# Kernel optimization log

Measured on AMD Instinct MI355X. Metric: run time of the kernel, lower is better.

The kernel has to match this reference:

```python
import jax, jax.numpy as jnp
import numpy as np

B, N, C, H, HD, HH, WW, K, ALPHA = 8, 4096, 256, 8, 32, 64, 64, 5, 4.0


def setup_inputs() -> dict:
    key = jax.random.key(0)
    ks = jax.random.split(key, 6)
    return {
        "x": jax.random.normal(ks[0], (B, N, C), jnp.float32),
        "W_qg": jax.random.normal(ks[1], (C, 2 * C), jnp.float32) * 0.02,
        "W_kv": jax.random.normal(ks[2], (C, 2 * C), jnp.float32) * 0.02,
        "W_proj": jax.random.normal(ks[3], (C, C), jnp.float32) * 0.02,
        "b_proj": jnp.zeros((C,), jnp.float32),
        "dwc_w": jax.random.normal(ks[4], (HD, 1, K, K), jnp.float32) * 0.05,
        "dwc_b": jnp.zeros((HD,), jnp.float32),
        "power_p": jnp.zeros((1, H, 1, HD), jnp.float32),
    }


def _safe_pow(x, p):
    # x >= 0 (post-relu). 0**p == 0 for p > 0; guard base so grads stay finite.
    xs = jnp.where(x > 0, x, 1.0)
    return jnp.where(x > 0, xs ** p, 0.0)


def reference(x, W_qg, W_kv, W_proj, b_proj, dwc_w, dwc_b, power_p):
    qg = x @ W_qg                                  # (B,N,2C)
    q, g = qg[..., :C], qg[..., C:]
    kv = x @ W_kv                                  # (B,N,2C)
    k = kv[..., :C].reshape(B, N, H, HD).transpose(0, 2, 1, 3)   # (B,H,N,hd)
    v = kv[..., C:].reshape(B, N, H, HD).transpose(0, 2, 1, 3)
    q = q.reshape(B, N, H, HD).transpose(0, 2, 1, 3)

    power = 1.0 + ALPHA * jax.nn.sigmoid(power_p)  # (1,H,1,hd)
    # x_s = q_pos@kv_s + q_neg@kv_s = (q_pos+q_neg)@kv_s, kv_s = (k_pos+k_neg)^T v_s
    q_sum = _safe_pow(jax.nn.relu(q), power) + _safe_pow(jax.nn.relu(-q), power)
    k_sum = _safe_pow(jax.nn.relu(k), power) + _safe_pow(jax.nn.relu(-k), power)

    v_s, v_o = v[..., : HD // 2], v[..., HD // 2 :]
    kv_s = jnp.einsum('bhnd,bhne->bhde', k_sum, v_s)
    kv_o = jnp.einsum('bhnd,bhne->bhde', k_sum, v_o)
    x_s = jnp.einsum('bhnd,bhde->bhne', q_sum, kv_s)
    x_o = jnp.einsum('bhnd,bhde->bhne', q_sum, kv_o)
    x_att = jnp.concatenate([x_s, x_o], -1).transpose(0, 2, 1, 3).reshape(B, N, C)

    # depthwise conv branch: exact layout replication of torch permute/reshape chain
    v_img = v.transpose(0, 2, 1, 3).reshape(B * H, HD, HH, WW)
    pad = K // 2
    v_loc = jax.lax.conv_general_dilated(
        v_img, dwc_w, (1, 1), [(pad, pad), (pad, pad)],
        feature_group_count=HD,
        dimension_numbers=('NCHW', 'OIHW', 'NCHW')) + dwc_b[None, :, None, None]
    v_loc = v_loc.reshape(B, H, HD, N).transpose(0, 2, 1, 3).reshape(B, C, N).transpose(0, 2, 1)

    return ((x_att + v_loc) * g) @ W_proj + b_proj
```

## Files before the change

kernel.cpp:

```cpp
#include <hip/hip_runtime.h>
#include <hip/hip_bf16.h>
#include <math.h>

#define B_ 8
#define N_ 4096
#define C_ 256
#define H_ 8
#define HD_ 32
#define BN_ (B_ * N_)
#define E_ ((size_t)BN_ * C_)

typedef __attribute__((ext_vector_type(8))) short short8;
typedef __attribute__((ext_vector_type(4))) float f32x4;

__device__ __forceinline__ float b2f(__hip_bfloat16 x) { return __bfloat162float(x); }

__device__ __forceinline__ void gl_lds16(const void* gp, void* lp) {
    __builtin_amdgcn_global_load_lds(
        (const __attribute__((address_space(1))) unsigned int*)gp,
        (__attribute__((address_space(3))) unsigned int*)lp,
        16, 0, 0);
}

__device__ __forceinline__ float fast_abspow(float v, float p) {
    float av = fabsf(v);
    return (av > 0.f) ? __builtin_amdgcn_exp2f(p * __builtin_amdgcn_logf(av)) : 0.f;
}

__device__ __forceinline__ float bf_lo(unsigned u) { return __uint_as_float(u << 16); }
__device__ __forceinline__ float bf_hi(unsigned u) { return __uint_as_float(u & 0xffff0000u); }
__device__ __forceinline__ unsigned short f2bfbits(float f) {
    __hip_bfloat16 h = __float2bfloat16(f);
    return *(unsigned short*)&h;
}
__device__ __forceinline__ unsigned pack2(float lo, float hi) {
    return (unsigned)f2bfbits(lo) | ((unsigned)f2bfbits(hi) << 16);
}

__global__ __launch_bounds__(256) void cvt_all(
    const float* __restrict__ x, const float* __restrict__ Wqg,
    const float* __restrict__ Wkv, const float* __restrict__ Wp,
    const float* __restrict__ pp,
    __hip_bfloat16* __restrict__ xb, __hip_bfloat16* __restrict__ Wt1,
    __hip_bfloat16* __restrict__ Wt2, float* __restrict__ powers)
{
    int t = threadIdx.x;
    int bid0 = blockIdx.x;
    if (bid0 < 4096) {
        size_t i = ((size_t)bid0 * 256 + t) * 8;
        float4 a = *(const float4*)&x[i];
        float4 b = *(const float4*)&x[i + 4];
        uint4 o = {pack2(a.x, a.y), pack2(a.z, a.w), pack2(b.x, b.y), pack2(b.z, b.w)};
        *(uint4*)&xb[i] = o;
        return;
    }
    int bid = bid0 - 4096;
    if (bid == 80) {
        powers[t] = 1.0f + 4.0f / (1.0f + expf(-pp[t]));
        return;
    }
    __shared__ float tile[64][65];
    const float* src;
    __hip_bfloat16* dst;
    int scols, tr, tc, dn0;
    if (bid < 32)      { src = Wqg; scols = 512; tr = bid >> 3;        tc = bid & 7;        dst = Wt1; dn0 = tc * 64; }
    else if (bid < 64) { src = Wkv; scols = 512; tr = (bid - 32) >> 3; tc = (bid - 32) & 7; dst = Wt1; dn0 = 512 + tc * 64; }
    else               { src = Wp;  scols = 256; tr = (bid - 64) >> 2; tc = (bid - 64) & 3; dst = Wt2; dn0 = tc * 64; }
    int tx = t & 63, ty = t >> 6;
    #pragma unroll
    for (int i = 0; i < 16; i++) {
        int r = ty + i * 4;
        tile[r][tx] = src[(size_t)(tr * 64 + r) * scols + tc * 64 + tx];
    }
    __syncthreads();
    #pragma unroll
    for (int i = 0; i < 16; i++) {
        int n_local = ty + i * 4;
        dst[(size_t)(dn0 + n_local) * 256 + tr * 64 + tx] = __float2bfloat16(tile[tx][n_local]);
    }
}

__global__ __launch_bounds__(256) void gemm1_mfma(
    const __hip_bfloat16* __restrict__ xb, const __hip_bfloat16* __restrict__ Wt1,
    const float* __restrict__ powers,
    __hip_bfloat16* __restrict__ q16, __hip_bfloat16* __restrict__ k16,
    __hip_bfloat16* __restrict__ g16, __hip_bfloat16* __restrict__ v16)
{
    __shared__ __align__(16) unsigned short As[2 * 128 * 32];
    __shared__ __align__(16) unsigned short Bs[2 * 128 * 32];
    int t = threadIdx.x;
    int w = t >> 6, l = t & 63;
    int row0 = blockIdx.x * 128;
    int col0 = blockIdx.y * 128;
    int wm = (w >> 1) * 64, wn = (w & 1) * 64;
    int lane15 = l & 15, quad = l >> 4;
    int srow = l >> 2;
    int skcol = (l & 3) * 8;

    f32x4 acc[4][4];
    #pragma unroll
    for (int mi = 0; mi < 4; mi++)
        #pragma unroll
        for (int ni = 0; ni < 4; ni++) acc[mi][ni] = (f32x4){0.f, 0.f, 0.f, 0.f};

    for (int k0 = 0; k0 < 256; k0 += 64) {
        #pragma unroll
        for (int kh = 0; kh < 2; kh++) {
            #pragma unroll
            for (int i = 0; i < 2; i++) {
                int r = i * 64 + w * 16 + srow;
                int kc = k0 + kh * 32 + skcol;
                gl_lds16(&xb[(size_t)(row0 + r) * 256 + kc],
                         &As[kh * 4096 + (i * 64 + w * 16) * 32]);
                gl_lds16(&Wt1[(size_t)(col0 + r) * 256 + kc],
                         &Bs[kh * 4096 + (i * 64 + w * 16) * 32]);
            }
        }
        __syncthreads();
        #pragma unroll
        for (int kh = 0; kh < 2; kh++) {
            short8 a[4], b[4];
            #pragma unroll
            for (int mi = 0; mi < 4; mi++)
                a[mi] = *(const short8*)&As[kh * 4096 + (wm + mi * 16 + lane15) * 32 + quad * 8];
            #pragma unroll
            for (int ni = 0; ni < 4; ni++)
                b[ni] = *(const short8*)&Bs[kh * 4096 + (wn + ni * 16 + lane15) * 32 + quad * 8];
            #pragma unroll
            for (int mi = 0; mi < 4; mi++)
                #pragma unroll
                for (int ni = 0; ni < 4; ni++)
                    acc[mi][ni] = __builtin_amdgcn_mfma_f32_16x16x32_bf16(a[mi], b[ni], acc[mi][ni], 0, 0, 0);
        }
        __syncthreads();
    }

    int region = blockIdx.y >> 1;
    bool dopow = (region == 0) || (region == 2);
    __hip_bfloat16* dst = (region == 0) ? q16 : (region == 1) ? g16 : (region == 2) ? k16 : v16;
    #pragma unroll
    for (int mi = 0; mi < 4; mi++) {
        #pragma unroll
        for (int ni = 0; ni < 4; ni++) {
            int row = row0 + wm + mi * 16 + quad * 4;
            int col = col0 + wn + ni * 16 + lane15;
            int c255 = col & 255;
            float p = powers[c255];
            #pragma unroll
            for (int r = 0; r < 4; r++) {
                float v = acc[mi][ni][r];
                float o = dopow ? fast_abspow(v, p) : v;
                dst[(size_t)(row + r) * 256 + c255] = __float2bfloat16(o);
            }
        }
    }
}

__global__ __launch_bounds__(256) void kvmat_kernel(
    const __hip_bfloat16* __restrict__ k16, const __hip_bfloat16* __restrict__ v16,
    float* __restrict__ kv_part)
{
    __shared__ __align__(16) unsigned short Kl[16 * 256];
    __shared__ __align__(16) unsigned short Vl[16 * 256];
    int t = threadIdx.x;
    int bid = blockIdx.x;
    int b = bid >> 5, seg = bid & 31;
    int h = t >> 5;
    float acc[32];
    #pragma unroll
    for (int e = 0; e < 32; e++) acc[e] = 0.f;
    const size_t base = (size_t)b * N_ * 256;
    int row = t >> 4, colb = (t & 15) * 16;
    for (int n0 = seg * 128; n0 < seg * 128 + 128; n0 += 16) {
        const uint4* ks = (const uint4*)(k16 + base + (size_t)(n0 + row) * 256 + colb);
        uint4 ka = ks[0], kb = ks[1];
        const uint4* vs = (const uint4*)(v16 + base + (size_t)(n0 + row) * 256 + colb);
        uint4 va = vs[0], vb = vs[1];
        __syncthreads();
        uint4* kd4 = (uint4*)&Kl[row * 256 + colb];
        kd4[0] = ka; kd4[1] = kb;
        uint4* vd4 = (uint4*)&Vl[row * 256 + colb];
        vd4[0] = va; vd4[1] = vb;
        __syncthreads();
        #pragma unroll
        for (int nn = 0; nn < 16; nn++) {
            float kd = bf_lo((unsigned)Kl[nn * 256 + t]);
            const uint4* vp = (const uint4*)&Vl[nn * 256 + h * 32];
            uint4 v0 = vp[0], v1 = vp[1], v2 = vp[2], v3 = vp[3];
            unsigned us[16] = {v0.x, v0.y, v0.z, v0.w, v1.x, v1.y, v1.z, v1.w,
                               v2.x, v2.y, v2.z, v2.w, v3.x, v3.y, v3.z, v3.w};
            #pragma unroll
            for (int j = 0; j < 16; j++) {
                acc[2 * j]     += kd * bf_lo(us[j]);
                acc[2 * j + 1] += kd * bf_hi(us[j]);
            }
        }
    }
    float* dst = kv_part + (size_t)bid * 8192;
    #pragma unroll
    for (int e = 0; e < 32; e++) dst[e * 256 + t] = acc[e];
}

__global__ __launch_bounds__(256) void kv_reduce(
    const float* __restrict__ kv_part, float* __restrict__ kv_mat2)
{
    int bid = blockIdx.x, t = threadIdx.x;
    int b = bid >> 3, chunk = bid & 7;
    #pragma unroll
    for (int j = 0; j < 4; j++) {
        int i = chunk * 1024 + j * 256 + t;
        float s = 0.f;
        for (int seg = 0; seg < 32; seg++)
            s += kv_part[((size_t)b * 32 + seg) * 8192 + i];
        kv_mat2[(size_t)b * 8192 + i] = s;
    }
}

__global__ __launch_bounds__(256) void conv_kernel(
    const __hip_bfloat16* __restrict__ v16,
    const float* __restrict__ w, const float* __restrict__ bias,
    __hip_bfloat16* __restrict__ vloc)
{
    __shared__ __align__(16) float img[64 * 72];
    __shared__ float wl[25];
    int t = threadIdx.x;
    int gid = blockIdx.x;
    int DD = gid & 31;
    if (t < 128) {
        int row = t >> 1, side = (t & 1) * 68;
        *(float4*)&img[row * 72 + side] = (float4){0.f, 0.f, 0.f, 0.f};
    }
    if (t < 25) wl[t] = w[DD * 25 + t];
    {
        int row = t >> 2, colb = (t & 3) * 16;
        const uint4* src = (const uint4*)(v16 + (size_t)gid * 4096 + row * 64 + colb);
        uint4 u0 = src[0], u1 = src[1];
        float4* d = (float4*)&img[row * 72 + 4 + colb];
        d[0] = (float4){bf_lo(u0.x), bf_hi(u0.x), bf_lo(u0.y), bf_hi(u0.y)};
        d[1] = (float4){bf_lo(u0.z), bf_hi(u0.z), bf_lo(u0.w), bf_hi(u0.w)};
        d[2] = (float4){bf_lo(u1.x), bf_hi(u1.x), bf_lo(u1.y), bf_hi(u1.y)};
        d[3] = (float4){bf_lo(u1.z), bf_hi(u1.z), bf_lo(u1.w), bf_hi(u1.w)};
    }
    __syncthreads();
    float bs = bias[DD];
    int x0 = (t & 15) * 4, yb = t >> 4;
    #pragma unroll
    for (int s = 0; s < 4; s++) {
        int y = yb + s * 16;
        float a0 = bs, a1 = bs, a2 = bs, a3 = bs;
        #pragma unroll
        for (int ky = 0; ky < 5; ky++) {
            int row = y + ky - 2;
            if (row < 0 || row >= 64) continue;
            const float* rp = &img[row * 72 + x0];
            float4 w0 = *(const float4*)rp;
            float4 w1 = *(const float4*)(rp + 4);
            float4 w2 = *(const float4*)(rp + 8);
            float win[12] = {w0.x, w0.y, w0.z, w0.w, w1.x, w1.y, w1.z, w1.w,
                             w2.x, w2.y, w2.z, w2.w};
            #pragma unroll
            for (int kx = 0; kx < 5; kx++) {
                float wt = wl[ky * 5 + kx];
                a0 += wt * win[2 + kx];
                a1 += wt * win[3 + kx];
                a2 += wt * win[4 + kx];
                a3 += wt * win[5 + kx];
            }
        }
        unsigned lo = pack2(a0, a1);
        unsigned hi = pack2(a2, a3);
        *(uint2*)(vloc + (size_t)gid * 4096 + y * 64 + x0) = (uint2){lo, hi};
    }
}

#define A2P 264
__global__ __launch_bounds__(256) void att_gemm2(
    const __hip_bfloat16* __restrict__ q16, const float* __restrict__ kv_mat2,
    const __hip_bfloat16* __restrict__ vloc, const __hip_bfloat16* __restrict__ g16,
    const __hip_bfloat16* __restrict__ Wt2, const float* __restrict__ bp,
    float* __restrict__ out)
{
    __shared__ __align__(16) unsigned short QA[64 * A2P];
    __shared__ __align__(16) unsigned short Bs[256 * 32];
    int t = threadIdx.x;
    int w = t >> 6, l = t & 63;
    int r0 = blockIdx.x * 64;
    int b = r0 >> 12, n0 = r0 & 4095;
    int lane15 = l & 15, quad = l >> 4;
    int h0 = w * 2;

    {
        const uint4* qsrc = (const uint4*)(q16 + (size_t)(r0 + (t >> 2)) * 256 + (t & 3) * 64);
        uint4* qdst = (uint4*)&QA[(t >> 2) * A2P + (t & 3) * 64];
        #pragma unroll
        for (int j = 0; j < 8; j++) qdst[j] = qsrc[j];
    }
    __syncthreads();

    short8 afr[4][2];
    #pragma unroll
    for (int m = 0; m < 4; m++)
        #pragma unroll
        for (int hh = 0; hh < 2; hh++)
            afr[m][hh] = *(const short8*)&QA[(m * 16 + lane15) * A2P + (h0 + hh) * 32 + quad * 8];

    short8 bfr[2][2];
    #pragma unroll
    for (int hh = 0; hh < 2; hh++) {
        #pragma unroll
        for (int nt = 0; nt < 2; nt++) {
            const float4* kp = (const float4*)(kv_mat2 + (size_t)b * 8192 +
                (size_t)(nt * 16 + lane15) * 256 + (h0 + hh) * 32 + quad * 8);
            float4 ka = kp[0], kb = kp[1];
            short8 bb;
            bb[0] = (short)f2bfbits(ka.x); bb[1] = (short)f2bfbits(ka.y);
            bb[2] = (short)f2bfbits(ka.z); bb[3] = (short)f2bfbits(ka.w);
            bb[4] = (short)f2bfbits(kb.x); bb[5] = (short)f2bfbits(kb.y);
            bb[6] = (short)f2bfbits(kb.z); bb[7] = (short)f2bfbits(kb.w);
            bfr[hh][nt] = bb;
        }
    }

    f32x4 ac[4][2][2];
    #pragma unroll
    for (int m = 0; m < 4; m++)
        #pragma unroll
        for (int hh = 0; hh < 2; hh++)
            #pragma unroll
            for (int nt = 0; nt < 2; nt++)
                ac[m][hh][nt] = __builtin_amdgcn_mfma_f32_16x16x32_bf16(
                    afr[m][hh], bfr[hh][nt], (f32x4){0.f, 0.f, 0.f, 0.f}, 0, 0, 0);

    #pragma unroll
    for (int m = 0; m < 4; m++) {
        #pragma unroll
        for (int hh = 0; hh < 2; hh++) {
            #pragma unroll
            for (int nt = 0; nt < 2; nt++) {
                int col = (h0 + hh) * 32 + nt * 16 + lane15;
                int rowb = m * 16 + quad * 4;
                size_t img = ((size_t)((b * 8 + (col & 7)) * 32 + (col >> 3))) * 4096 + n0 + rowb;
                uint2 vv = *(const uint2*)(vloc + img);
                float vl[4] = {bf_lo(vv.x), bf_hi(vv.x), bf_lo(vv.y), bf_hi(vv.y)};
                #pragma unroll
                for (int i = 0; i < 4; i++) {
                    float gg = b2f(g16[(size_t)(r0 + rowb + i) * 256 + col]);
                    float val = (ac[m][hh][nt][i] + vl[i]) * gg;
                    QA[(rowb + i) * A2P + col] = f2bfbits(val);
                }
            }
        }
    }

    int wm = (w & 1) * 32, wn = (w >> 1) * 128;
    f32x4 acc2[2][8];
    #pragma unroll
    for (int mi = 0; mi < 2; mi++)
        #pragma unroll
        for (int ni = 0; ni < 8; ni++) acc2[mi][ni] = (f32x4){0.f, 0.f, 0.f, 0.f};

    for (int k0 = 0; k0 < 256; k0 += 32) {
        __syncthreads();
        #pragma unroll
        for (int i = 0; i < 4; i++) {
            int ncol = i * 64 + w * 16 + (l >> 2);
            gl_lds16(&Wt2[(size_t)ncol * 256 + k0 + (l & 3) * 8],
                     &Bs[(i * 64 + w * 16) * 32]);
        }
        __syncthreads();
        short8 a[2], bb[8];
        #pragma unroll
        for (int mi = 0; mi < 2; mi++)
            a[mi] = *(const short8*)&QA[(wm + mi * 16 + lane15) * A2P + k0 + quad * 8];
        #pragma unroll
        for (int ni = 0; ni < 8; ni++)
            bb[ni] = *(const short8*)&Bs[(wn + ni * 16 + lane15) * 32 + quad * 8];
        #pragma unroll
        for (int mi = 0; mi < 2; mi++)
            #pragma unroll
            for (int ni = 0; ni < 8; ni++)
                acc2[mi][ni] = __builtin_amdgcn_mfma_f32_16x16x32_bf16(a[mi], bb[ni], acc2[mi][ni], 0, 0, 0);
    }

    #pragma unroll
    for (int mi = 0; mi < 2; mi++) {
        #pragma unroll
        for (int ni = 0; ni < 8; ni++) {
            int row = r0 + wm + mi * 16 + quad * 4;
            int col = wn + ni * 16 + lane15;
            float bv = bp[col];
            #pragma unroll
            for (int r = 0; r < 4; r++)
                out[(size_t)(row + r) * 256 + col] = acc2[mi][ni][r] + bv;
        }
    }
}

extern "C" void kernel_launch(void* const* d_in, const int* in_sizes, int n_in,
                              void* d_out, int out_size, void* d_ws, size_t ws_size,
                              hipStream_t stream) {
    const float* x      = (const float*)d_in[0];
    const float* W_qg   = (const float*)d_in[1];
    const float* W_kv   = (const float*)d_in[2];
    const float* W_proj = (const float*)d_in[3];
    const float* b_proj = (const float*)d_in[4];
    const float* dwc_w  = (const float*)d_in[5];
    const float* dwc_b  = (const float*)d_in[6];
    const float* pow_p  = (const float*)d_in[7];
    float* out = (float*)d_out;

    float* ws = (float*)d_ws;
    const size_t E = E_;
    __hip_bfloat16* q16  = (__hip_bfloat16*)ws;
    __hip_bfloat16* k16  = (__hip_bfloat16*)(ws + E / 2);
    __hip_bfloat16* g16  = (__hip_bfloat16*)(ws + E);
    __hip_bfloat16* v16  = (__hip_bfloat16*)(ws + 3 * E / 2);
    __hip_bfloat16* xb   = (__hip_bfloat16*)(ws + 2 * E);
    __hip_bfloat16* vl16 = (__hip_bfloat16*)(ws + 5 * E / 2);
    float* kv_part = ws + 3 * E;
    float* kv_mat2 = kv_part + 256 * 8192;
    __hip_bfloat16* Wt1 = (__hip_bfloat16*)(kv_mat2 + 65536);
    __hip_bfloat16* Wt2 = Wt1 + 262144;
    float* powers = (float*)(Wt2 + 65536);

    cvt_all<<<4096 + 81, 256, 0, stream>>>(x, W_qg, W_kv, W_proj, pow_p, xb, Wt1, Wt2, powers);
    gemm1_mfma<<<dim3(BN_ / 128, 8), 256, 0, stream>>>(xb, Wt1, powers, q16, k16, g16, v16);
    kvmat_kernel<<<256, 256, 0, stream>>>(k16, v16, kv_part);
    kv_reduce<<<64, 256, 0, stream>>>(kv_part, kv_mat2);
    conv_kernel<<<2048, 256, 0, stream>>>(v16, dwc_w, dwc_b, vl16);
    att_gemm2<<<512, 256, 0, stream>>>(q16, kv_mat2, vl16, g16, Wt2, b_proj, out);
}
```

Baseline: 199.1 us.

## Merge kv-matrix and conv kernels, reduce kv partials via atomics, swizzle gemm1 blocks

```diff
diff --git a/kernel.cpp b/kernel.cpp
--- a/kernel.cpp
+++ b/kernel.cpp
@@ -42,7 +42,8 @@
     const float* __restrict__ Wkv, const float* __restrict__ Wp,
     const float* __restrict__ pp,
     __hip_bfloat16* __restrict__ xb, __hip_bfloat16* __restrict__ Wt1,
-    __hip_bfloat16* __restrict__ Wt2, float* __restrict__ powers)
+    __hip_bfloat16* __restrict__ Wt2, float* __restrict__ powers,
+    float* __restrict__ kv_mat2)
 {
     int t = threadIdx.x;
     int bid0 = blockIdx.x;
@@ -59,6 +60,10 @@
         powers[t] = 1.0f + 4.0f / (1.0f + expf(-pp[t]));
         return;
     }
+    if (bid >= 81) {
+        ((float4*)kv_mat2)[(size_t)(bid - 81) * 256 + t] = (float4){0.f, 0.f, 0.f, 0.f};
+        return;
+    }
     __shared__ float tile[64][65];
     const float* src;
     __hip_bfloat16* dst;
@@ -90,8 +95,10 @@
     __shared__ __align__(16) unsigned short Bs[2 * 128 * 32];
     int t = threadIdx.x;
     int w = t >> 6, l = t & 63;
-    int row0 = blockIdx.x * 128;
-    int col0 = blockIdx.y * 128;
+    int bswz = (blockIdx.x & 7) * 256 + (blockIdx.x >> 3);
+    int row0 = (bswz >> 3) * 128;
+    int colb = bswz & 7;
+    int col0 = colb * 128;
     int wm = (w >> 1) * 64, wn = (w & 1) * 64;
     int lane15 = l & 15, quad = l >> 4;
     int srow = l >> 2;
@@ -135,7 +142,7 @@
         __syncthreads();
     }
 
-    int region = blockIdx.y >> 1;
+    int region = colb >> 1;
     bool dopow = (region == 0) || (region == 2);
     __hip_bfloat16* dst = (region == 0) ? q16 : (region == 1) ? g16 : (region == 2) ? k16 : v16;
     #pragma unroll
@@ -156,75 +163,60 @@
     }
 }
 
-__global__ __launch_bounds__(256) void kvmat_kernel(
+__global__ __launch_bounds__(256) void kvconv_kernel(
     const __hip_bfloat16* __restrict__ k16, const __hip_bfloat16* __restrict__ v16,
-    float* __restrict__ kv_part)
-{
-    __shared__ __align__(16) unsigned short Kl[16 * 256];
-    __shared__ __align__(16) unsigned short Vl[16 * 256];
-    int t = threadIdx.x;
-    int bid = blockIdx.x;
-    int b = bid >> 5, seg = bid & 31;
-    int h = t >> 5;
-    float acc[32];
-    #pragma unroll
-    for (int e = 0; e < 32; e++) acc[e] = 0.f;
-    const size_t base = (size_t)b * N_ * 256;
-    int row = t >> 4, colb = (t & 15) * 16;
-    for (int n0 = seg * 128; n0 < seg * 128 + 128; n0 += 16) {
-        const uint4* ks = (const uint4*)(k16 + base + (size_t)(n0 + row) * 256 + colb);
-        uint4 ka = ks[0], kb = ks[1];
-        const uint4* vs = (const uint4*)(v16 + base + (size_t)(n0 + row) * 256 + colb);
-        uint4 va = vs[0], vb = vs[1];
-        __syncthreads();
-        uint4* kd4 = (uint4*)&Kl[row * 256 + colb];
-        kd4[0] = ka; kd4[1] = kb;
-        uint4* vd4 = (uint4*)&Vl[row * 256 + colb];
-        vd4[0] = va; vd4[1] = vb;
-        __syncthreads();
-        #pragma unroll
-        for (int nn = 0; nn < 16; nn++) {
-            float kd = bf_lo((unsigned)Kl[nn * 256 + t]);
-            const uint4* vp = (const uint4*)&Vl[nn * 256 + h * 32];
-            uint4 v0 = vp[0], v1 = vp[1], v2 = vp[2], v3 = vp[3];
-            unsigned us[16] = {v0.x, v0.y, v0.z, v0.w, v1.x, v1.y, v1.z, v1.w,
-                               v2.x, v2.y, v2.z, v2.w, v3.x, v3.y, v3.z, v3.w};
-            #pragma unroll
-            for (int j = 0; j < 16; j++) {
-                acc[2 * j]     += kd * bf_lo(us[j]);
-                acc[2 * j + 1] += kd * bf_hi(us[j]);
-            }
-        }
-    }
-    float* dst = kv_part + (size_t)bid * 8192;
-    #pragma unroll
-    for (int e = 0; e < 32; e++) dst[e * 256 + t] = acc[e];
-}
-
-__global__ __launch_bounds__(256) void kv_reduce(
-    const float* __restrict__ kv_part, float* __restrict__ kv_mat2)
-{
-    int bid = blockIdx.x, t = threadIdx.x;
-    int b = bid >> 3, chunk = bid & 7;
-    #pragma unroll
-    for (int j = 0; j < 4; j++) {
-        int i = chunk * 1024 + j * 256 + t;
-        float s = 0.f;
-        for (int seg = 0; seg < 32; seg++)
-            s += kv_part[((size_t)b * 32 + seg) * 8192 + i];
-        kv_mat2[(size_t)b * 8192 + i] = s;
-    }
-}
-
-__global__ __launch_bounds__(256) void conv_kernel(
-    const __hip_bfloat16* __restrict__ v16,
+    float* __restrict__ kv_mat2,
     const float* __restrict__ w, const float* __restrict__ bias,
     __hip_bfloat16* __restrict__ vloc)
 {
-    __shared__ __align__(16) float img[64 * 72];
-    __shared__ float wl[25];
+    __shared__ __align__(16) unsigned char smraw[64 * 72 * 4 + 128];
     int t = threadIdx.x;
-    int gid = blockIdx.x;
+
+    if (blockIdx.x < 256) {
+        unsigned short* Kl = (unsigned short*)smraw;
+        unsigned short* Vl = (unsigned short*)(smraw + 8192);
+        int bid = blockIdx.x;
+        int b = bid >> 5, seg = bid & 31;
+        int h = t >> 5;
+        float acc[32];
+        #pragma unroll
+        for (int e = 0; e < 32; e++) acc[e] = 0.f;
+        const size_t base = (size_t)b * N_ * 256;
+        int row = t >> 4, colb = (t & 15) * 16;
+        for (int n0 = seg * 128; n0 < seg * 128 + 128; n0 += 16) {
+            const uint4* ks = (const uint4*)(k16 + base + (size_t)(n0 + row) * 256 + colb);
+            uint4 ka = ks[0], kb = ks[1];
+            const uint4* vs = (const uint4*)(v16 + base + (size_t)(n0 + row) * 256 + colb);
+            uint4 va = vs[0], vb = vs[1];
+            __syncthreads();
+            uint4* kd4 = (uint4*)&Kl[row * 256 + colb];
+            kd4[0] = ka; kd4[1] = kb;
+            uint4* vd4 = (uint4*)&Vl[row * 256 + colb];
+            vd4[0] = va; vd4[1] = vb;
+            __syncthreads();
+            #pragma unroll
+            for (int nn = 0; nn < 16; nn++) {
+                float kd = bf_lo((unsigned)Kl[nn * 256 + t]);
+                const uint4* vp = (const uint4*)&Vl[nn * 256 + h * 32];
+                uint4 v0 = vp[0], v1 = vp[1], v2 = vp[2], v3 = vp[3];
+                unsigned us[16] = {v0.x, v0.y, v0.z, v0.w, v1.x, v1.y, v1.z, v1.w,
+                                   v2.x, v2.y, v2.z, v2.w, v3.x, v3.y, v3.z, v3.w};
+                #pragma unroll
+                for (int j = 0; j < 16; j++) {
+                    acc[2 * j]     += kd * bf_lo(us[j]);
+                    acc[2 * j + 1] += kd * bf_hi(us[j]);
+                }
+            }
+        }
+        float* dst = kv_mat2 + (size_t)b * 8192;
+        #pragma unroll
+        for (int e = 0; e < 32; e++) atomicAdd(&dst[e * 256 + t], acc[e]);
+        return;
+    }
+
+    float* img = (float*)smraw;
+    float* wl  = (float*)(smraw + 64 * 72 * 4);
+    int gid = blockIdx.x - 256;
     int DD = gid & 31;
     if (t < 128) {
         int row = t >> 1, side = (t & 1) * 68;
@@ -423,10 +415,8 @@
     __hip_bfloat16* Wt2 = Wt1 + 262144;
     float* powers = (float*)(Wt2 + 65536);
 
-    cvt_all<<<4096 + 81, 256, 0, stream>>>(x, W_qg, W_kv, W_proj, pow_p, xb, Wt1, Wt2, powers);
-    gemm1_mfma<<<dim3(BN_ / 128, 8), 256, 0, stream>>>(xb, Wt1, powers, q16, k16, g16, v16);
-    kvmat_kernel<<<256, 256, 0, stream>>>(k16, v16, kv_part);
-    kv_reduce<<<64, 256, 0, stream>>>(kv_part, kv_mat2);
-    conv_kernel<<<2048, 256, 0, stream>>>(v16, dwc_w, dwc_b, vl16);
+    cvt_all<<<4096 + 81 + 64, 256, 0, stream>>>(x, W_qg, W_kv, W_proj, pow_p, xb, Wt1, Wt2, powers, kv_mat2);
+    gemm1_mfma<<<2048, 256, 0, stream>>>(xb, Wt1, powers, q16, k16, g16, v16);
+    kvconv_kernel<<<256 + 2048, 256, 0, stream>>>(k16, v16, kv_mat2, dwc_w, dwc_b, vl16);
     att_gemm2<<<512, 256, 0, stream>>>(q16, kv_mat2, vl16, g16, Wt2, b_proj, out);
 }
```

Measured after the change: 205.2 us. 3.0% more time.
